# Kernel tuning notes

Measured on AMD Instinct MI355X. Metric: run time of the kernel, lower is better.

## Reference

```python
import jax, jax.numpy as jnp
import numpy as np

N_QUBITS = 6      # 4 data + 2 ancilla
N_DATA = 4
N_LAYERS = 4
N_GROUPS = 8
DIM = 2 ** N_QUBITS  # 64 statevector amplitudes (real: RY + CNOT keep state real)
GN_GROUPS = 32
EPS = 1e-5


def _cnot_ring_perm():
    # CNOT(q, q+1 mod n) ring applied sequentially; compose into one basis permutation.
    n = N_QUBITS
    f = np.arange(DIM)
    for c in range(n):
        t = (c + 1) % n
        cbit = (f >> (n - 1 - c)) & 1
        f = np.where(cbit == 1, f ^ (1 << (n - 1 - t)), f)
    # new_state[f[i]] = old_state[i]  =>  new = old[finv]
    finv = np.empty(DIM, dtype=np.int64)
    finv[f] = np.arange(DIM)
    return jnp.asarray(finv)


def _zsign():
    i = np.arange(DIM)[:, None]
    q = np.arange(N_DATA)[None, :]
    return jnp.asarray(1.0 - 2.0 * ((i >> (N_QUBITS - 1 - q)) & 1), dtype=jnp.float32)


PERM = _cnot_ring_perm()
ZSIGN = _zsign()


def _group_norm(x, gamma, beta):
    B, C, H, W = x.shape
    xg = x.reshape(B, GN_GROUPS, C // GN_GROUPS, H, W)
    mu = xg.mean(axis=(2, 3, 4), keepdims=True)
    var = xg.var(axis=(2, 3, 4), keepdims=True)
    xn = ((xg - mu) * jax.lax.rsqrt(var + EPS)).reshape(B, C, H, W)
    return xn * gamma[None, :, None, None] + beta[None, :, None, None]


def _apply_ry(state, half_angle, q):
    # state: [B,H,W,G,64]; half_angle: [B,H,W,G]; RY = [[c,-s],[s,c]] on qubit q
    pre, post = 2 ** q, 2 ** (N_QUBITS - 1 - q)
    s = state.reshape(state.shape[:-1] + (pre, 2, post))
    c = jnp.cos(half_angle)[..., None, None]
    sn = jnp.sin(half_angle)[..., None, None]
    a0, a1 = s[..., 0, :], s[..., 1, :]
    new = jnp.stack([c * a0 - sn * a1, sn * a0 + c * a1], axis=-2)
    return new.reshape(state.shape)


def _forward(x, emb, gamma, beta, w_in, b_in, theta, w_style, b_style, w_out, b_out):
    B, C, H, W = x.shape
    h = _group_norm(x, gamma, beta)                       # norm0
    emb_a = emb * jax.nn.sigmoid(emb)                     # SiLU(emb)
    # 1x1 projection to per-group data-qubit rotation angles: [B,H,W,G,4]
    ang = jnp.einsum('oc,bchw->bohw', w_in, h) + b_in[None, :, None, None]
    ang = ang.reshape(B, N_GROUPS, N_DATA, H, W).transpose(0, 3, 4, 1, 2)
    # style modulation of circuit parameters: [B,G,L,Q]
    style = (emb_a @ w_style.T + b_style).reshape(B, N_GROUPS, N_LAYERS, N_QUBITS)
    # init |0...0> per pixel per group
    state = jnp.zeros((B, H, W, N_GROUPS, DIM), x.dtype).at[..., 0].set(1.0)
    for l in range(N_LAYERS):
        for q in range(N_QUBITS):
            a = theta[:, l, q][None, None, None, :] + style[:, :, l, q][:, None, None, :]
            if q < N_DATA:                                # data reuploading each layer
                a = a + ang[..., q]
            state = _apply_ry(state, 0.5 * a, q)
        state = state[..., PERM]                          # CNOT ring entangler
    probs = state * state
    meas = probs @ ZSIGN                                  # [B,H,W,G,4] <Z> on data qubits
    meas = meas.transpose(0, 3, 4, 1, 2).reshape(B, N_GROUPS * N_DATA, H, W)
    out = jnp.einsum('oc,bchw->bohw', w_out, meas) + b_out[None, :, None, None]
    return out + x                                        # residual


def setup_inputs() -> dict:
    key = jax.random.key(0)
    ks = jax.random.split(key, 6)
    B, C, H, W, E = 16, 256, 32, 32, 512
    return {
        'x': jax.random.normal(ks[0], (B, C, H, W), jnp.float32),
        'emb': jax.random.normal(ks[1], (B, E), jnp.float32),
        'gamma': jnp.ones((C,), jnp.float32),
        'beta': jnp.zeros((C,), jnp.float32),
        'w_in': jax.random.normal(ks[2], (32, C), jnp.float32) * 0.1,
        'b_in': jnp.zeros((32,), jnp.float32),
        'theta': jax.random.normal(ks[3], (N_GROUPS, N_LAYERS, N_QUBITS), jnp.float32) * 0.5,
        'w_style': jax.random.normal(ks[4], (N_GROUPS * N_LAYERS * N_QUBITS, E), jnp.float32) * 0.02,
        'b_style': jnp.zeros((N_GROUPS * N_LAYERS * N_QUBITS,), jnp.float32),
        'w_out': jax.random.normal(ks[5], (C, 32), jnp.float32) * 0.05,
        'b_out': jnp.zeros((C,), jnp.float32),
    }


def reference(x, emb, gamma, beta, w_in, b_in, theta, w_style, b_style, w_out, b_out):
    return _forward(x, emb, gamma, beta, w_in, b_in, theta, w_style, b_style, w_out, b_out)
```

## Files before the change

### kernel.cpp

```cpp
#include <hip/hip_runtime.h>
#include <math.h>

#define NB 16
#define NC 256
#define NHW 1024
#define NE 512
#define NDQ 4
#define NLQ 4
#define NQB 6
#define QDIM 64
#define PIX 16
#define HSS 264

typedef float v2f __attribute__((ext_vector_type(2)));
typedef float f32x4 __attribute__((ext_vector_type(4)));
typedef short bf16x8 __attribute__((ext_vector_type(8)));

__device__ __forceinline__ short f2bf(float v) {
    unsigned u = __builtin_bit_cast(unsigned, v);
    u += 0x7FFFu + ((u >> 16) & 1u);
    return (short)(u >> 16);
}

constexpr int fwd1(int i) {
    int r = i;
    for (int c = 0; c < NQB; ++c) {
        int t = (c + 1) % NQB;
        if ((r >> (NQB - 1 - c)) & 1) r ^= 1 << (NQB - 1 - t);
    }
    return r;
}
constexpr int fwdl(int s, int l) { for (int i = 0; i < l; ++i) s = fwd1(s); return s; }
constexpr int parity6(int x) { x ^= x >> 4; x ^= x >> 2; x ^= x >> 1; return x & 1; }

struct GateTab { int M[NLQ][NQB]; int V[NLQ][NQB]; int W[NDQ]; };
constexpr GateTab make_tab() {
    GateTab g{};
    for (int l = 0; l < NLQ; ++l)
        for (int q = 0; q < NQB; ++q) {
            int m = 1 << (NQB - 1 - q);
            for (int x = 0; x < QDIM; ++x) if (fwdl(x, l) == m) { g.M[l][q] = x; break; }
            int V = 0;
            for (int t = 0; t < NQB; ++t) V |= ((fwdl(1 << t, l) >> (NQB - 1 - q)) & 1) << t;
            g.V[l][q] = V;
        }
    for (int d = 0; d < NDQ; ++d) {
        int W = 0;
        for (int t = 0; t < NQB; ++t) W |= ((fwdl(1 << t, NLQ) >> (NQB - 1 - d)) & 1) << t;
        g.W[d] = W;
    }
    return g;
}
constexpr GateTab GT = make_tab();

__global__ __launch_bounds__(256) void k_pre(const float* __restrict__ x,
                                             const float* __restrict__ emb,
                                             const float* __restrict__ w_style,
                                             const float* __restrict__ b_style,
                                             const float* __restrict__ theta,
                                             const float* __restrict__ w_in,
                                             const float* __restrict__ w_out,
                                             const float* __restrict__ gamma,
                                             const float* __restrict__ beta,
                                             float* __restrict__ scs,
                                             float* __restrict__ shs,
                                             float* __restrict__ A,
                                             short* __restrict__ wbf) {
    if (blockIdx.x < 512) {
        int bg = blockIdx.x;
        const float4* xp = (const float4*)(x + (size_t)bg * 8 * NHW);
        float s = 0.f, ss = 0.f;
        for (int i = threadIdx.x; i < 8 * NHW / 4; i += 256) {
            float4 v = xp[i];
            s  += v.x + v.y + v.z + v.w;
            ss += v.x*v.x + v.y*v.y + v.z*v.z + v.w*v.w;
        }
        __shared__ float red0[4], red1[4];
        #pragma unroll
        for (int o = 32; o; o >>= 1) { s += __shfl_down(s, o); ss += __shfl_down(ss, o); }
        int lane = threadIdx.x & 63, w = threadIdx.x >> 6;
        if (lane == 0) { red0[w] = s; red1[w] = ss; }
        __syncthreads();
        if (threadIdx.x == 0) {
            s  = red0[0] + red0[1] + red0[2] + red0[3];
            ss = red1[0] + red1[1] + red1[2] + red1[3];
            float m = s * (1.f / 8192.f);
            float rsv = rsqrtf(ss * (1.f / 8192.f) - m * m + 1e-5f);
            int cbase = (bg & 31) * 8;
            int b = bg >> 5;
            #pragma unroll
            for (int j = 0; j < 8; ++j) {
                int c = cbase + j;
                float sc = rsv * gamma[c];
                scs[b * NC + c] = sc;
                shs[b * NC + c] = fmaf(-m, sc, beta[c]);
            }
        }
    } else if (blockIdx.x < 512 + NB) {
        int b = blockIdx.x - 512;
        __shared__ float es[NE];
        int t = threadIdx.x;
        for (int i = t; i < NE; i += 256) {
            float v = emb[b * NE + i];
            es[i] = v / (1.f + __expf(-v));
        }
        __syncthreads();
        int j0 = t >> 3, sub = t & 7;
        for (int pass = 0; pass < 6; ++pass) {
            int j = pass * 32 + j0;
            const float* wr = w_style + (size_t)j * NE + sub * 64;
            const float* er = es + sub * 64;
            float acc = 0.f;
            #pragma unroll
            for (int i = 0; i < 64; i += 4) {
                float4 w4 = *(const float4*)(wr + i);
                acc = fmaf(w4.x, er[i],   acc);
                acc = fmaf(w4.y, er[i+1], acc);
                acc = fmaf(w4.z, er[i+2], acc);
                acc = fmaf(w4.w, er[i+3], acc);
            }
            acc += __shfl_xor(acc, 1);
            acc += __shfl_xor(acc, 2);
            acc += __shfl_xor(acc, 4);
            if (sub == 0) A[b * 192 + j] = theta[j] + b_style[j] + acc;
        }
    } else {
        for (int i = threadIdx.x; i < 8192; i += 256) wbf[i] = f2bf(w_in[i]);
        for (int i = threadIdx.x; i < 8192; i += 256) wbf[8192 + i] = f2bf(w_out[i]);
    }
}

__global__ __launch_bounds__(256, 2) void k_main(
    const float* __restrict__ x,
    const float* __restrict__ scs,
    const float* __restrict__ shs,
    const float* __restrict__ b_in,
    const float* __restrict__ A,
    const short* __restrict__ w_in_bf,
    const short* __restrict__ w_out_bf,
    const float* __restrict__ b_out,
    float* __restrict__ out) {

    __shared__ short hs[PIX * HSS];
    __shared__ float xs2[NC * PIX];
    __shared__ float as_[PIX * 36];

    int blk = blockIdx.x;
    int b = blk >> 6;
    int pbase = (blk & 63) * PIX;
    int t = threadIdx.x;
    int lane = t & 63, wv = t >> 6;
    int c0 = t >> 2, f4 = (t & 3) * 4;
    int nn = lane & 15, quad = lane >> 4;

    float4 xr[4];
    #pragma unroll
    for (int k = 0; k < 4; ++k) {
        int c = c0 + 64 * k;
        xr[k] = *(const float4*)(x + (size_t)(b * NC + c) * NHW + pbase + f4);
        *(float4*)(xs2 + c * PIX + f4) = xr[k];
    }

    bf16x8 bfrag[8];
    if (wv >= 2) {
        int o = ((wv - 2) << 4) + nn;
        #pragma unroll
        for (int s = 0; s < 8; ++s)
            bfrag[s] = *(const bf16x8*)(w_in_bf + o * NC + s * 32 + quad * 8);
    }

    float Ar[24];
    if (wv < 2) {
        int g = (t & 127) >> 4;
        const float4* Ab4 = (const float4*)(A + b * 192 + g * 24);
        #pragma unroll
        for (int j = 0; j < 6; ++j) {
            float4 a4 = Ab4[j];
            Ar[4*j] = a4.x; Ar[4*j+1] = a4.y; Ar[4*j+2] = a4.z; Ar[4*j+3] = a4.w;
        }
    }

    #pragma unroll
    for (int k = 0; k < 4; ++k) {
        int c = c0 + 64 * k;
        float sc = scs[b * NC + c];
        float sh = shs[b * NC + c];
        float4 v = xr[k];
        hs[(f4 + 0) * HSS + c] = f2bf(fmaf(v.x, sc, sh));
        hs[(f4 + 1) * HSS + c] = f2bf(fmaf(v.y, sc, sh));
        hs[(f4 + 2) * HSS + c] = f2bf(fmaf(v.z, sc, sh));
        hs[(f4 + 3) * HSS + c] = f2bf(fmaf(v.w, sc, sh));
    }
    __syncthreads();

    if (wv >= 2) {
        f32x4 acc = {0.f, 0.f, 0.f, 0.f};
        #pragma unroll
        for (int s = 0; s < 8; ++s) {
            bf16x8 afr = *(const bf16x8*)(hs + nn * HSS + s * 32 + quad * 8);
            acc = __builtin_amdgcn_mfma_f32_16x16x32_bf16(afr, bfrag[s], acc, 0, 0, 0);
        }
        int o = ((wv - 2) << 4) + nn;
        float bi = b_in[o];
        #pragma unroll
        for (int r = 0; r < 4; ++r)
            as_[(quad * 4 + r) * 36 + o] = acc[r] + bi;
    }

    bf16x8 bfr4[4];
    float  bo4[4];
    #pragma unroll
    for (int ti = 0; ti < 4; ++ti) {
        int c = (wv * 4 + ti) * 16 + nn;
        bfr4[ti] = *(const bf16x8*)(w_out_bf + c * 32 + quad * 8);
        bo4[ti]  = b_out[c];
    }
    __syncthreads();

    if (t < 128) {
        int g = t >> 4, p = t & 15;
        float4 angv = *(const float4*)(as_ + p * 36 + g * 4);
        float angp[NDQ] = {angv.x, angv.y, angv.z, angv.w};

        v2f st2[32];
        #pragma unroll
        for (int k = 0; k < 32; ++k) st2[k] = (v2f){0.f, 0.f};
        st2[0].x = 1.f;

        #pragma unroll
        for (int l = 0; l < NLQ; ++l) {
            #pragma unroll
            for (int q = 0; q < NQB; ++q) {
                const int M = GT.M[l][q], V = GT.V[l][q];
                const int KD = M >> 1, SW = M & 1;
                int hh = KD; hh |= hh >> 1; hh |= hh >> 2; hh |= hh >> 4;
                const int HB = hh - (hh >> 1);
                float a = Ar[l * NQB + q] + (q < NDQ ? angp[q] : 0.f);
                float sn, cs;
                __sincosf(0.5f * a, &sn, &cs);
                v2f cs2 = {cs, cs};
                v2f sPP = {sn, sn}, sPM = {sn, -sn}, sMP = {-sn, sn}, sMM = {-sn, -sn};
                auto COV = [&](int i0) -> v2f {
                    bool p0 = parity6(i0 & V), p1 = parity6((i0 + 1) & V);
                    return p0 ? (p1 ? sPP : sPM) : (p1 ? sMP : sMM);
                };
                if (KD == 0) {
                    #pragma unroll
                    for (int k = 0; k < 32; ++k) {
                        v2f ov = __builtin_shufflevector(st2[k], st2[k], 1, 0);
                        st2[k] = __builtin_elementwise_fma(COV(2*k), ov, cs2 * st2[k]);
                    }
                } else {
                    #pragma unroll
                    for (int k = 0; k < 32; ++k) {
                        if (k & HB) continue;
                        int kp = k ^ KD;
                        v2f av = st2[k], bv = st2[kp];
                        v2f am = SW ? __builtin_shufflevector(av, av, 1, 0) : av;
                        v2f bm = SW ? __builtin_shufflevector(bv, bv, 1, 0) : bv;
                        st2[k]  = __builtin_elementwise_fma(COV(2*k),  bm, cs2 * av);
                        st2[kp] = __builtin_elementwise_fma(COV(2*kp), am, cs2 * bv);
                    }
                }
            }
        }

        #pragma unroll
        for (int k = 0; k < 32; ++k) st2[k] = st2[k] * st2[k];
        float md[NDQ];
        #pragma unroll
        for (int d = 0; d < NDQ; ++d) {
            const int W = GT.W[d];
            v2f acc = {0.f, 0.f};
            #pragma unroll
            for (int k = 0; k < 32; ++k) {
                v2f sg = { parity6((2*k)     & W) ? -1.f : 1.f,
                           parity6((2*k + 1) & W) ? -1.f : 1.f };
                acc = __builtin_elementwise_fma(sg, st2[k], acc);
            }
            md[d] = acc.x + acc.y;
        }
        float4 mv = {md[0], md[1], md[2], md[3]};
        *(float4*)(as_ + p * 36 + g * 4) = mv;
    }
    __syncthreads();

    {
        float4 m0 = *(const float4*)(as_ + nn * 36 + quad * 8);
        float4 m1 = *(const float4*)(as_ + nn * 36 + quad * 8 + 4);
        bf16x8 afr = { f2bf(m0.x), f2bf(m0.y), f2bf(m0.z), f2bf(m0.w),
                       f2bf(m1.x), f2bf(m1.y), f2bf(m1.z), f2bf(m1.w) };
        #pragma unroll
        for (int ti = 0; ti < 4; ++ti) {
            int c = (wv * 4 + ti) * 16 + nn;
            f32x4 acc = {0.f, 0.f, 0.f, 0.f};
            acc = __builtin_amdgcn_mfma_f32_16x16x32_bf16(afr, bfr4[ti], acc, 0, 0, 0);
            float4 x4 = *(const float4*)(xs2 + c * PIX + quad * 4);
            float4 r;
            r.x = acc[0] + bo4[ti] + x4.x;
            r.y = acc[1] + bo4[ti] + x4.y;
            r.z = acc[2] + bo4[ti] + x4.z;
            r.w = acc[3] + bo4[ti] + x4.w;
            *(float4*)(out + (size_t)(b * NC + c) * NHW + pbase + quad * 4) = r;
        }
    }
}

extern "C" void kernel_launch(void* const* d_in, const int* in_sizes, int n_in,
                              void* d_out, int out_size, void* d_ws, size_t ws_size,
                              hipStream_t stream) {
    const float* x       = (const float*)d_in[0];
    const float* emb     = (const float*)d_in[1];
    const float* gamma   = (const float*)d_in[2];
    const float* beta    = (const float*)d_in[3];
    const float* w_in    = (const float*)d_in[4];
    const float* b_in    = (const float*)d_in[5];
    const float* theta   = (const float*)d_in[6];
    const float* w_style = (const float*)d_in[7];
    const float* b_style = (const float*)d_in[8];
    const float* w_out   = (const float*)d_in[9];
    const float* b_out   = (const float*)d_in[10];
    float* out = (float*)d_out;

    float* ws  = (float*)d_ws;
    float* scs = ws;
    float* shs = ws + 4096;
    float* A   = ws + 8192;
    short* wbf = (short*)(ws + 12288);

    k_pre<<<512 + NB + 1, 256, 0, stream>>>(x, emb, w_style, b_style, theta,
                                            w_in, w_out, gamma, beta,
                                            scs, shs, A, wbf);
    k_main<<<NB * 64, 256, 0, stream>>>(x, scs, shs, b_in, A,
                                        wbf, wbf + 8192, b_out, out);
}
```

Before: 120.5 us.

## Double pixels per block so all four waves share GEMM and circuit work

Raises the per-block pixel tile from 16 to 32 and halves the grid. All four waves now take part in the input projection MFMA, with a 2x2 split over pixel and output tiles, and all 256 threads run the quantum circuit simulation instead of only 128. Each weight fragment and style parameter load is amortized over twice as many pixels. In exchange, LDS use per block roughly doubles and the grid drops to 512 blocks on a 256-CU device, which may lower occupancy and latency hiding.

```diff
diff --git a/kernel.cpp b/kernel.cpp
--- a/kernel.cpp
+++ b/kernel.cpp
@@ -9,7 +9,7 @@
 #define NLQ 4
 #define NQB 6
 #define QDIM 64
-#define PIX 16
+#define PIX 32
 #define HSS 264
 
 typedef float v2f __attribute__((ext_vector_type(2)));
@@ -146,32 +146,33 @@
     __shared__ float as_[PIX * 36];
 
     int blk = blockIdx.x;
-    int b = blk >> 6;
-    int pbase = (blk & 63) * PIX;
+    int b = blk >> 5;
+    int pbase = (blk & 31) * PIX;
     int t = threadIdx.x;
     int lane = t & 63, wv = t >> 6;
-    int c0 = t >> 2, f4 = (t & 3) * 4;
+    int c0 = t >> 3, p4 = (t & 7) * 4;
     int nn = lane & 15, quad = lane >> 4;
-
-    float4 xr[4];
+    int mt = wv >> 1, nt = wv & 1;
+
+    float4 xr[8];
     #pragma unroll
-    for (int k = 0; k < 4; ++k) {
-        int c = c0 + 64 * k;
-        xr[k] = *(const float4*)(x + (size_t)(b * NC + c) * NHW + pbase + f4);
-        *(float4*)(xs2 + c * PIX + f4) = xr[k];
+    for (int k = 0; k < 8; ++k) {
+        int c = c0 + 32 * k;
+        xr[k] = *(const float4*)(x + (size_t)(b * NC + c) * NHW + pbase + p4);
+        *(float4*)(xs2 + c * PIX + p4) = xr[k];
     }
 
     bf16x8 bfrag[8];
-    if (wv >= 2) {
-        int o = ((wv - 2) << 4) + nn;
+    {
+        int o = nt * 16 + nn;
         #pragma unroll
         for (int s = 0; s < 8; ++s)
             bfrag[s] = *(const bf16x8*)(w_in_bf + o * NC + s * 32 + quad * 8);
     }
 
     float Ar[24];
-    if (wv < 2) {
-        int g = (t & 127) >> 4;
+    {
+        int g = t >> 5;
         const float4* Ab4 = (const float4*)(A + b * 192 + g * 24);
         #pragma unroll
         for (int j = 0; j < 6; ++j) {
@@ -181,30 +182,30 @@
     }
 
     #pragma unroll
-    for (int k = 0; k < 4; ++k) {
-        int c = c0 + 64 * k;
+    for (int k = 0; k < 8; ++k) {
+        int c = c0 + 32 * k;
         float sc = scs[b * NC + c];
         float sh = shs[b * NC + c];
         float4 v = xr[k];
-        hs[(f4 + 0) * HSS + c] = f2bf(fmaf(v.x, sc, sh));
-        hs[(f4 + 1) * HSS + c] = f2bf(fmaf(v.y, sc, sh));
-        hs[(f4 + 2) * HSS + c] = f2bf(fmaf(v.z, sc, sh));
-        hs[(f4 + 3) * HSS + c] = f2bf(fmaf(v.w, sc, sh));
+        hs[(p4 + 0) * HSS + c] = f2bf(fmaf(v.x, sc, sh));
+        hs[(p4 + 1) * HSS + c] = f2bf(fmaf(v.y, sc, sh));
+        hs[(p4 + 2) * HSS + c] = f2bf(fmaf(v.z, sc, sh));
+        hs[(p4 + 3) * HSS + c] = f2bf(fmaf(v.w, sc, sh));
     }
     __syncthreads();
 
-    if (wv >= 2) {
+    {
         f32x4 acc = {0.f, 0.f, 0.f, 0.f};
         #pragma unroll
         for (int s = 0; s < 8; ++s) {
-            bf16x8 afr = *(const bf16x8*)(hs + nn * HSS + s * 32 + quad * 8);
+            bf16x8 afr = *(const bf16x8*)(hs + (mt * 16 + nn) * HSS + s * 32 + quad * 8);
             acc = __builtin_amdgcn_mfma_f32_16x16x32_bf16(afr, bfrag[s], acc, 0, 0, 0);
         }
-        int o = ((wv - 2) << 4) + nn;
+        int o = nt * 16 + nn;
         float bi = b_in[o];
         #pragma unroll
         for (int r = 0; r < 4; ++r)
-            as_[(quad * 4 + r) * 36 + o] = acc[r] + bi;
+            as_[(mt * 16 + quad * 4 + r) * 36 + o] = acc[r] + bi;
     }
 
     bf16x8 bfr4[4];
@@ -217,8 +218,8 @@
     }
     __syncthreads();
 
-    if (t < 128) {
-        int g = t >> 4, p = t & 15;
+    {
+        int g = t >> 5, p = t & 31;
         float4 angv = *(const float4*)(as_ + p * 36 + g * 4);
         float angp[NDQ] = {angv.x, angv.y, angv.z, angv.w};
 
@@ -285,9 +286,10 @@
     }
     __syncthreads();
 
-    {
-        float4 m0 = *(const float4*)(as_ + nn * 36 + quad * 8);
-        float4 m1 = *(const float4*)(as_ + nn * 36 + quad * 8 + 4);
+    #pragma unroll
+    for (int pt = 0; pt < 2; ++pt) {
+        float4 m0 = *(const float4*)(as_ + (pt * 16 + nn) * 36 + quad * 8);
+        float4 m1 = *(const float4*)(as_ + (pt * 16 + nn) * 36 + quad * 8 + 4);
         bf16x8 afr = { f2bf(m0.x), f2bf(m0.y), f2bf(m0.z), f2bf(m0.w),
                        f2bf(m1.x), f2bf(m1.y), f2bf(m1.z), f2bf(m1.w) };
         #pragma unroll
@@ -295,13 +297,13 @@
             int c = (wv * 4 + ti) * 16 + nn;
             f32x4 acc = {0.f, 0.f, 0.f, 0.f};
             acc = __builtin_amdgcn_mfma_f32_16x16x32_bf16(afr, bfr4[ti], acc, 0, 0, 0);
-            float4 x4 = *(const float4*)(xs2 + c * PIX + quad * 4);
+            float4 x4 = *(const float4*)(xs2 + c * PIX + pt * 16 + quad * 4);
             float4 r;
             r.x = acc[0] + bo4[ti] + x4.x;
             r.y = acc[1] + bo4[ti] + x4.y;
             r.z = acc[2] + bo4[ti] + x4.z;
             r.w = acc[3] + bo4[ti] + x4.w;
-            *(float4*)(out + (size_t)(b * NC + c) * NHW + pbase + quad * 4) = r;
+            *(float4*)(out + (size_t)(b * NC + c) * NHW + pbase + pt * 16 + quad * 4) = r;
         }
     }
 }
@@ -331,6 +333,6 @@
     k_pre<<<512 + NB + 1, 256, 0, stream>>>(x, emb, w_style, b_style, theta,
                                             w_in, w_out, gamma, beta,
                                             scs, shs, A, wbf);
-    k_main<<<NB * 64, 256, 0, stream>>>(x, scs, shs, b_in, A,
+    k_main<<<NB * 32, 256, 0, stream>>>(x, scs, shs, b_in, A,
                                         wbf, wbf + 8192, b_out, out);
 }
```

Measured after the change: 119.0 us. Within noise of the previous version (-1.3%).
